# Kernel tuning notes

Hardware: AMD Instinct MI355X
Metric: run time of the kernel (lower is better)

The kernel has to match this reference:

```python
import jax, jax.numpy as jnp
import numpy as np

D = 512
H = 8
HD = D // H
EPS = 1e-5
NEG_INF = -1e30


def _ln(x, g, b):
    mu = jnp.mean(x, axis=-1, keepdims=True)
    var = jnp.mean(jnp.square(x - mu), axis=-1, keepdims=True)
    return (x - mu) * jax.lax.rsqrt(var + EPS) * g + b


def setup_inputs() -> dict:
    key = jax.random.key(0)
    ks = jax.random.split(key, 8)
    V, M, S = 128, 128, 514  # seq includes 2 head tokens (cls+dist)
    inp = {
        "video_embeds": jax.random.normal(ks[0], (V, D), jnp.float32),
        "music_features": jax.random.normal(ks[1], (M, S, D), jnp.float32),
        "music_masks": jnp.ones((M, S - 2), jnp.int32),
    }
    wk = jax.random.split(ks[2], 5)
    for name, k in zip(["Wq", "Wk", "Wv", "Wo", "Wl"], wk):
        inp[name] = jax.random.normal(k, (D, D), jnp.float32) * 0.02
    for name in ["bq", "bk", "bv", "bo", "bl"]:
        inp[name] = jnp.zeros((D,), jnp.float32)
    for name in ["g1", "g2", "g3"]:
        inp[name] = jnp.ones((D,), jnp.float32)
    for name in ["b1", "b2", "b3"]:
        inp[name] = jnp.zeros((D,), jnp.float32)
    return inp


def reference(video_embeds, music_features, music_masks,
              Wq, bq, Wk, bk, Wv, bv, Wo, bo, Wl, bl,
              g1, b1, g2, b2, g3, b3):
    # drop cls + dist tokens
    mf = music_features[:, 2:, :]  # (M, f, D)
    ve = _ln(video_embeds, g1, b1)  # (V, D)
    mf = _ln(mf, g1, b1)
    V = ve.shape[0]
    M, f, _ = mf.shape

    q = (ve @ Wq.T + bq).reshape(V, H, HD).transpose(1, 0, 2)        # (H, V, hd)
    k = (mf @ Wk.T + bk).reshape(M, f, H, HD).transpose(0, 2, 1, 3)  # (M, H, f, hd)
    v = (mf @ Wv.T + bv).reshape(M, f, H, HD).transpose(0, 2, 1, 3)  # (M, H, f, hd)

    logits = jnp.einsum('hvd,mhfd->vmhf', q, k) / np.sqrt(HD).astype(np.float32)
    mask = music_masks[None, :, None, :]  # (1, M, 1, f)
    logits = jnp.where(mask == 0, NEG_INF, logits)
    w = jax.nn.softmax(logits, axis=-1)
    attn = jnp.einsum('vmhf,mhfd->vmhd', w, v).reshape(V, M, D)
    attn = attn @ Wo.T + bo

    attn = _ln(attn, g2, b2)
    out = attn + (attn @ Wl.T + bl)  # dropout = identity in eval
    return _ln(out, g3, b3)
```

## Files before the change

kernel.cpp:

```cpp
#include <hip/hip_runtime.h>
#include <hip/hip_bf16.h>

typedef unsigned int uint;
typedef unsigned short ushort;
typedef __bf16 bf16;
typedef bf16 bf16x8 __attribute__((ext_vector_type(8)));
typedef float f32x4 __attribute__((ext_vector_type(4)));
typedef ushort ushort4v __attribute__((ext_vector_type(4)));

__device__ __forceinline__ float bf2f(ushort u) {
  union { uint u; float f; } v; v.u = ((uint)u) << 16; return v.f;
}
__device__ __forceinline__ ushort f2bf(float f) {
  union { float f; uint u; } v; v.f = f;
  uint u = v.u;
  uint r = (u + 0x7fffu + ((u >> 16) & 1u)) >> 16;
  return (ushort)r;
}

__device__ __forceinline__ void gl2lds16(const void* g, void* l) {
  __builtin_amdgcn_global_load_lds(
      (const __attribute__((address_space(1))) void*)g,
      (__attribute__((address_space(3))) void*)l, 16, 0, 0);
}

__device__ __forceinline__ void ln_rows0(
    int nrows, int blk, int nblk, int tid,
    const float* __restrict__ srcA,
    const float* __restrict__ g, const float* __restrict__ b,
    ushort* __restrict__ dst)
{
  const int l = tid & 63;
  const int nw = nblk * 4;
  for (int row = blk * 4 + (tid >> 6); row < nrows; row += nw) {
    const float* s = srcA + (size_t)row * 512;
    float x[8];
    float4 a0 = *(const float4*)(s + l * 4);
    float4 a1 = *(const float4*)(s + 256 + l * 4);
    x[0] = a0.x; x[1] = a0.y; x[2] = a0.z; x[3] = a0.w;
    x[4] = a1.x; x[5] = a1.y; x[6] = a1.z; x[7] = a1.w;
    float sum = 0.f, sq = 0.f;
    #pragma unroll
    for (int j = 0; j < 8; ++j) { sum += x[j]; sq += x[j] * x[j]; }
    #pragma unroll
    for (int o = 1; o < 64; o <<= 1) {
      sum += __shfl_xor(sum, o);
      sq  += __shfl_xor(sq, o);
    }
    float mu = sum * (1.f / 512.f);
    float var = sq * (1.f / 512.f) - mu * mu;
    float rstd = rsqrtf(var + 1e-5f);
    float4 g0 = *(const float4*)(g + l * 4);
    float4 g1 = *(const float4*)(g + 256 + l * 4);
    float4 b0 = *(const float4*)(b + l * 4);
    float4 b1 = *(const float4*)(b + 256 + l * 4);
    float gv[8] = {g0.x,g0.y,g0.z,g0.w,g1.x,g1.y,g1.z,g1.w};
    float bv[8] = {b0.x,b0.y,b0.z,b0.w,b1.x,b1.y,b1.z,b1.w};
    ushort* d = dst + (size_t)row * 512;
    ushort4v p0, p1;
    #pragma unroll
    for (int j = 0; j < 4; ++j) {
      p0[j] = f2bf((x[j] - mu) * rstd * gv[j] + bv[j]);
      p1[j] = f2bf((x[4+j] - mu) * rstd * gv[4+j] + bv[4+j]);
    }
    *(ushort4v*)(d + l * 4) = p0;
    *(ushort4v*)(d + 256 + l * 4) = p1;
  }
}

__device__ __forceinline__ void ln_pair1(
    int wid, int tid,
    const float* __restrict__ srcA,
    const float* __restrict__ g, const float* __restrict__ b,
    ushort* __restrict__ dst)
{
  const int l = tid & 63;
  const int r0 = wid * 2, r1 = r0 + 1;
  float x0[8], x1[8];
  int mm0 = r0 >> 9, fi0 = r0 & 511;
  int mm1 = r1 >> 9, fi1 = r1 & 511;
  const float* s0 = srcA + ((size_t)mm0 * 514 + 2 + fi0) * 512;
  const float* s1 = srcA + ((size_t)mm1 * 514 + 2 + fi1) * 512;
  float4 a0 = *(const float4*)(s0 + l * 4);
  float4 a1 = *(const float4*)(s0 + 256 + l * 4);
  float4 c0 = *(const float4*)(s1 + l * 4);
  float4 c1 = *(const float4*)(s1 + 256 + l * 4);
  x0[0]=a0.x; x0[1]=a0.y; x0[2]=a0.z; x0[3]=a0.w;
  x0[4]=a1.x; x0[5]=a1.y; x0[6]=a1.z; x0[7]=a1.w;
  x1[0]=c0.x; x1[1]=c0.y; x1[2]=c0.z; x1[3]=c0.w;
  x1[4]=c1.x; x1[5]=c1.y; x1[6]=c1.z; x1[7]=c1.w;
  float s0v = 0.f, q0 = 0.f, s1v = 0.f, q1 = 0.f;
  #pragma unroll
  for (int j = 0; j < 8; ++j) {
    s0v += x0[j]; q0 += x0[j] * x0[j];
    s1v += x1[j]; q1 += x1[j] * x1[j];
  }
  #pragma unroll
  for (int o = 1; o < 64; o <<= 1) {
    s0v += __shfl_xor(s0v, o); q0 += __shfl_xor(q0, o);
    s1v += __shfl_xor(s1v, o); q1 += __shfl_xor(q1, o);
  }
  float mu0 = s0v * (1.f/512.f), mu1 = s1v * (1.f/512.f);
  float rstd0 = rsqrtf(q0 * (1.f/512.f) - mu0 * mu0 + 1e-5f);
  float rstd1 = rsqrtf(q1 * (1.f/512.f) - mu1 * mu1 + 1e-5f);
  float4 g0 = *(const float4*)(g + l * 4);
  float4 g1v = *(const float4*)(g + 256 + l * 4);
  float4 b0 = *(const float4*)(b + l * 4);
  float4 b1v = *(const float4*)(b + 256 + l * 4);
  float gv[8] = {g0.x,g0.y,g0.z,g0.w,g1v.x,g1v.y,g1v.z,g1v.w};
  float bv[8] = {b0.x,b0.y,b0.z,b0.w,b1v.x,b1v.y,b1v.z,b1v.w};
  ushort* d0 = dst + (size_t)r0 * 512;
  ushort* d1 = dst + (size_t)r1 * 512;
  ushort4v p00, p01, p10, p11;
  #pragma unroll
  for (int j = 0; j < 4; ++j) {
    p00[j] = f2bf((x0[j]-mu0)*rstd0*gv[j]+bv[j]);
    p01[j] = f2bf((x0[4+j]-mu0)*rstd0*gv[4+j]+bv[4+j]);
    p10[j] = f2bf((x1[j]-mu1)*rstd1*gv[j]+bv[j]);
    p11[j] = f2bf((x1[4+j]-mu1)*rstd1*gv[4+j]+bv[4+j]);
  }
  *(ushort4v*)(d0 + l * 4) = p00;
  *(ushort4v*)(d0 + 256 + l * 4) = p01;
  *(ushort4v*)(d1 + l * 4) = p10;
  *(ushort4v*)(d1 + 256 + l * 4) = p11;
}

struct PreArgs {
  const float* s0; const float* s1; const float* s2; const float* s3; const float* s4;
  ushort* d0; ushort* d1; ushort* d2; ushort* d3; ushort* d4;
  const float* video; const float* music;
  const float* g1; const float* b1;
  ushort* veln; ushort* mfln;
};
__global__ __launch_bounds__(256) void preamble(PreArgs a) {
  int bb = blockIdx.x;
  if (bb < 640) {
    int t = bb * 256 + threadIdx.x;
    int which = t >> 15;
    int e = (t & 32767) * 8;
    const float* s = which == 0 ? a.s0 : which == 1 ? a.s1 : which == 2 ? a.s2 : which == 3 ? a.s3 : a.s4;
    ushort*      d = which == 0 ? a.d0 : which == 1 ? a.d1 : which == 2 ? a.d2 : which == 3 ? a.d3 : a.d4;
    float4 v0 = *(const float4*)(s + e);
    float4 v1 = *(const float4*)(s + e + 4);
    uint4 o;
    o.x = (uint)f2bf(v0.x) | ((uint)f2bf(v0.y) << 16);
    o.y = (uint)f2bf(v0.z) | ((uint)f2bf(v0.w) << 16);
    o.z = (uint)f2bf(v1.x) | ((uint)f2bf(v1.y) << 16);
    o.w = (uint)f2bf(v1.z) | ((uint)f2bf(v1.w) << 16);
    *(uint4*)(d + e) = o;
  } else if (bb < 672) {
    ln_rows0(128, bb - 640, 32, threadIdx.x, a.video, a.g1, a.b1, a.veln);
  } else {
    ln_pair1((bb - 672) * 4 + (threadIdx.x >> 6), threadIdx.x,
             a.music, a.g1, a.b1, a.mfln);
  }
}

__global__ __launch_bounds__(512) void gemm_kvq(
    const ushort* __restrict__ Amf, const ushort* __restrict__ Aq,
    const ushort* __restrict__ Wk, const ushort* __restrict__ Wv,
    const ushort* __restrict__ Wq,
    const float* __restrict__ bk, const float* __restrict__ bv,
    const float* __restrict__ bq,
    ushort* __restrict__ K, ushort* __restrict__ Vt, ushort* __restrict__ Q)
{
  __shared__ __align__(16) ushort As[2][256 * 64];
  __shared__ __align__(16) ushort Bks[2][128 * 64];
  __shared__ __align__(16) ushort Bvs[2][128 * 64];
  const int tid = threadIdx.x;
  const int w = tid >> 6, l = tid & 63;
  const int lg = l >> 4, lr = l & 15;
  const int wr = w >> 1, wc = w & 1;

  const bool isq = (blockIdx.y == 256);
  const int row0 = isq ? 0 : blockIdx.y * 256;
  const int col0 = blockIdx.x * 128;
  const ushort* Ap  = isq ? Aq : Amf;
  const ushort* Wkp = isq ? Wq : Wk;

  f32x4 kacc[4][4], vacc[4][4];
  #pragma unroll
  for (int i = 0; i < 4; i++)
    #pragma unroll
    for (int j = 0; j < 4; j++) {
      f32x4 z = {0.f,0.f,0.f,0.f};
      kacc[i][j] = z; vacc[i][j] = z;
    }

  size_t asrc[4], wksrc[2]; int aldst[4], wldst[2];
  {
    int r = tid >> 3, j = tid & 7;
    int koff = (j ^ (r & 7)) * 8;
    #pragma unroll
    for (int c2 = 0; c2 < 4; ++c2) {
      asrc[c2] = (size_t)(row0 + c2 * 64 + r) * 512 + koff;
      aldst[c2] = ((c2 * 64 + w * 8) * 64);
    }
    #pragma unroll
    for (int c2 = 0; c2 < 2; ++c2) {
      wksrc[c2] = (size_t)(col0 + c2 * 64 + r) * 512 + koff;
      wldst[c2] = ((c2 * 64 + w * 8) * 64);
    }
  }

  auto stage = [&](int pb, int kk) {
    #pragma unroll
    for (int c2 = 0; c2 < 4; ++c2)
      gl2lds16(Ap + asrc[c2] + kk * 64, &As[pb][aldst[c2]]);
    #pragma unroll
    for (int c2 = 0; c2 < 2; ++c2) {
      gl2lds16(Wkp + wksrc[c2] + kk * 64, &Bks[pb][wldst[c2]]);
      gl2lds16(Wv + wksrc[c2] + kk * 64, &Bvs[pb][wldst[c2]]);
    }
  };
  auto compute = [&](int pb) {
    #pragma unroll
    for (int ks = 0; ks < 2; ++ks) {
      bf16x8 af[4], bkf[4];
      #pragma unroll
      for (int mi = 0; mi < 4; ++mi) {
        int r = wr * 64 + mi * 16 + lr;
        af[mi] = *(const bf16x8*)(&As[pb][r * 64 + ((ks * 32 + lg * 8) ^ ((r & 7) * 8))]);
      }
      #pragma unroll
      for (int ni = 0; ni < 4; ++ni) {
        int r = wc * 64 + ni * 16 + lr;
        bkf[ni] = *(const bf16x8*)(&Bks[pb][r * 64 + ((ks * 32 + lg * 8) ^ ((r & 7) * 8))]);
      }
      #pragma unroll
      for (int mi = 0; mi < 4; ++mi)
        #pragma unroll
        for (int ni = 0; ni < 4; ++ni)
          kacc[mi][ni] = __builtin_amdgcn_mfma_f32_16x16x32_bf16(af[mi], bkf[ni], kacc[mi][ni], 0, 0, 0);
      if (!isq) {
        bf16x8 bvf[4];
        #pragma unroll
        for (int ni = 0; ni < 4; ++ni) {
          int r = wc * 64 + ni * 16 + lr;
          bvf[ni] = *(const bf16x8*)(&Bvs[pb][r * 64 + ((ks * 32 + lg * 8) ^ ((r & 7) * 8))]);
        }
        #pragma unroll
        for (int mi = 0; mi < 4; ++mi)
          #pragma unroll
          for (int ni = 0; ni < 4; ++ni)
            vacc[mi][ni] = __builtin_amdgcn_mfma_f32_16x16x32_bf16(af[mi], bvf[ni], vacc[mi][ni], 0, 0, 0);
      }
    }
  };

  stage(0, 0);
  __syncthreads();
  int cur = 0;
  #pragma unroll
  for (int kk = 0; kk < 7; ++kk) {
    stage(cur ^ 1, kk + 1);
    compute(cur);
    __syncthreads();
    cur ^= 1;
  }
  compute(cur);

  #pragma unroll
  for (int ni = 0; ni < 4; ++ni) {
    int cg = col0 + wc * 64 + ni * 16 + lr;
    float bkc = isq ? bq[cg] : bk[cg];
    float bvc = isq ? 0.f : bv[cg];
    #pragma unroll
    for (int mi = 0; mi < 4; ++mi) {
      int rg0 = row0 + wr * 64 + mi * 16 + lg * 4;
      if (isq) {
        if (rg0 < 128) {
          #pragma unroll
          for (int e = 0; e < 4; ++e)
            Q[(size_t)(rg0 + e) * 512 + cg] = f2bf((kacc[mi][ni][e] + bkc) * 0.125f);
        }
      } else {
        #pragma unroll
        for (int e = 0; e < 4; ++e)
          K[(size_t)(rg0 + e) * 512 + cg] = f2bf(kacc[mi][ni][e] + bkc);
        int m = rg0 >> 9, fi = rg0 & 511;
        ushort4v pk;
        #pragma unroll
        for (int e = 0; e < 4; ++e) pk[e] = f2bf(vacc[mi][ni][e] + bvc);
        *(ushort4v*)(Vt + (size_t)(m * 512 + cg) * 512 + fi) = pk;
      }
    }
  }
}

__global__ __launch_bounds__(512) void gemm_ln(
    const ushort* __restrict__ A, const ushort* __restrict__ W,
    const float* __restrict__ bias,
    const float* __restrict__ gam, const float* __restrict__ bet,
    void* __restrict__ outp, const ushort* __restrict__ resid, int outf32)
{
  __shared__ __align__(16) ushort As[2][64 * 64];
  __shared__ __align__(16) ushort Bs[2][512 * 64];
  __shared__ float red[8][64][2];
  const int tid = threadIdx.x;
  const int w = tid >> 6, l = tid & 63;
  const int lg = l >> 4, lr = l & 15;
  const int row0 = blockIdx.x * 64;

  f32x4 acc[4][4];
  #pragma unroll
  for (int i = 0; i < 4; i++)
    #pragma unroll
    for (int j = 0; j < 4; j++) { f32x4 z = {0.f,0.f,0.f,0.f}; acc[i][j] = z; }

  size_t asrc, wsrc0; int aldst;
  {
    int r = tid >> 3, j = tid & 7;
    int koff = (j ^ (r & 7)) * 8;
    asrc = (size_t)(row0 + r) * 512 + koff;
    wsrc0 = (size_t)r * 512 + koff;
    aldst = (w * 8) * 64;
  }

  auto stage = [&](int pb, int kk) {
    gl2lds16(A + asrc + kk * 64, &As[pb][aldst]);
    #pragma unroll
    for (int b = 0; b < 8; ++b)
      gl2lds16(W + wsrc0 + (size_t)b * 32768 + kk * 64,
               &Bs[pb][(b * 64 + w * 8) * 64]);
  };
  auto compute = [&](int pb) {
    #pragma unroll
    for (int ks = 0; ks < 2; ++ks) {
      bf16x8 af[4], bfr[4];
      #pragma unroll
      for (int mi = 0; mi < 4; ++mi) {
        int ra = mi * 16 + lr;
        af[mi] = *(const bf16x8*)(&As[pb][ra * 64 + ((ks * 32 + lg * 8) ^ ((ra & 7) * 8))]);
      }
      #pragma unroll
      for (int ni = 0; ni < 4; ++ni) {
        int rb = w * 64 + ni * 16 + lr;
        bfr[ni] = *(const bf16x8*)(&Bs[pb][rb * 64 + ((ks * 32 + lg * 8) ^ ((rb & 7) * 8))]);
      }
      __builtin_amdgcn_s_setprio(1);
      #pragma unroll
      for (int mi = 0; mi < 4; ++mi)
        #pragma unroll
        for (int ni = 0; ni < 4; ++ni)
          acc[mi][ni] = __builtin_amdgcn_mfma_f32_16x16x32_bf16(af[mi], bfr[ni], acc[mi][ni], 0, 0, 0);
      __builtin_amdgcn_s_setprio(0);
    }
  };

  stage(0, 0);
  __syncthreads();
  int cur = 0;
  #pragma unroll
  for (int kk = 0; kk < 7; ++kk) {
    stage(cur ^ 1, kk + 1);
    compute(cur);
    __syncthreads();
    cur ^= 1;
  }
  compute(cur);

  float bc[4], gv[4], bv2[4];
  #pragma unroll
  for (int ni = 0; ni < 4; ++ni) {
    int col = w * 64 + ni * 16 + lr;
    bc[ni] = bias[col];
    gv[ni] = gam[col];
    bv2[ni] = bet[col];
  }
  #pragma unroll
  for (int mi = 0; mi < 4; ++mi)
    #pragma unroll
    for (int e = 0; e < 4; ++e) {
      int row = row0 + mi * 16 + lg * 4 + e;
      #pragma unroll
      for (int ni = 0; ni < 4; ++ni) {
        float v = acc[mi][ni][e] + bc[ni];
        if (resid) v += bf2f(resid[(size_t)row * 512 + w * 64 + ni * 16 + lr]);
        acc[mi][ni][e] = v;
      }
    }
  #pragma unroll
  for (int mi = 0; mi < 4; ++mi)
    #pragma unroll
    for (int e = 0; e < 4; ++e) {
      float s = acc[mi][0][e] + acc[mi][1][e] + acc[mi][2][e] + acc[mi][3][e];
      float q = acc[mi][0][e]*acc[mi][0][e] + acc[mi][1][e]*acc[mi][1][e]
              + acc[mi][2][e]*acc[mi][2][e] + acc[mi][3][e]*acc[mi][3][e];
      #pragma unroll
      for (int o = 1; o < 16; o <<= 1) { s += __shfl_xor(s, o); q += __shfl_xor(q, o); }
      if (lr == 0) {
        int row = mi * 16 + lg * 4 + e;
        red[w][row][0] = s;
        red[w][row][1] = q;
      }
    }
  __syncthreads();
  #pragma unroll
  for (int mi = 0; mi < 4; ++mi)
    #pragma unroll
    for (int e = 0; e < 4; ++e) {
      int row = mi * 16 + lg * 4 + e;
      float S = 0.f, Qm = 0.f;
      #pragma unroll
      for (int w2 = 0; w2 < 8; ++w2) { S += red[w2][row][0]; Qm += red[w2][row][1]; }
      float mu = S * (1.f / 512.f);
      float var = Qm * (1.f / 512.f) - mu * mu;
      float rstd = rsqrtf(var + 1e-5f);
      int grow = row0 + row;
      if (!outf32) {
        ushort* o = (ushort*)outp;
        #pragma unroll
        for (int ni = 0; ni < 4; ++ni)
          o[(size_t)grow * 512 + w * 64 + ni * 16 + lr] =
              f2bf((acc[mi][ni][e] - mu) * rstd * gv[ni] + bv2[ni]);
      } else {
        float* o = (float*)outp;
        #pragma unroll
        for (int ni = 0; ni < 4; ++ni)
          o[(size_t)grow * 512 + w * 64 + ni * 16 + lr] =
              (acc[mi][ni][e] - mu) * rstd * gv[ni] + bv2[ni];
      }
    }
}

__global__ __launch_bounds__(256) void attn_kernel(
    const ushort* __restrict__ q, const ushort* __restrict__ k,
    const ushort* __restrict__ vt, const int* __restrict__ masks,
    ushort* __restrict__ attn)
{
  __shared__ __align__(16) ushort Qs[128 * 64];
  __shared__ __align__(16) ushort Ks[2][64 * 64];
  __shared__ __align__(16) ushort Vs[2][64 * 64];
  __shared__ __align__(16) ushort Ps[4][32 * 64];
  __shared__ float maskf[2][64];
  __shared__ float stats[4][32];

  const int tid = threadIdx.x;
  const int w = tid >> 6, l = tid & 63;
  const int lg = l >> 4, lr = l & 15;
  const int m = blockIdx.x >> 3, h = blockIdx.x & 7;

  const size_t kbase = (size_t)(m * 512) * 512 + h * 64;
  const size_t vbase = (size_t)(m * 512 + h * 64) * 512;

  auto stageKV = [&](int pb, int it) {
    const int f0 = it * 64;
    #pragma unroll
    for (int c2 = 0; c2 < 2; ++c2) {
      int c = c2 * 256 + tid;
      int r = c >> 3, j = c & 7;
      int off = (j * 8) ^ ((r & 7) * 8);
      gl2lds16(k + kbase + (size_t)(f0 + r) * 512 + off, &Ks[pb][(c2 * 256 + w * 64) * 8]);
      gl2lds16(vt + vbase + (size_t)r * 512 + f0 + off, &Vs[pb][(c2 * 256 + w * 64) * 8]);
    }
    if (tid < 64) maskf[pb][tid] = masks[m * 512 + f0 + tid] ? 0.f : -1e30f;
  };

  #pragma unroll
  for (int c2 = 0; c2 < 4; ++c2) {
    int c = c2 * 256 + tid;
    int r = c >> 3, j = c & 7;
    gl2lds16(q + (size_t)r * 512 + h * 64 + ((j * 8) ^ ((r & 7) * 8)),
             Qs + (c2 * 256 + w * 64) * 8);
  }
  stageKV(0, 0);
  __syncthreads();

  f32x4 acc[2][4];
  #pragma unroll
  for (int i = 0; i < 2; i++)
    #pragma unroll
    for (int j = 0; j < 4; j++) { f32x4 z = {0.f,0.f,0.f,0.f}; acc[i][j] = z; }
  float m_run[2] = {-INFINITY, -INFINITY};
  float l_run[2] = {0.f, 0.f};
  bf16x8 qf[2][2];
  #pragma unroll
  for (int nv = 0; nv < 2; ++nv)
    #pragma unroll
    for (int k2 = 0; k2 < 2; ++k2) {
      int v = w * 32 + nv * 16 + lr;
      qf[nv][k2] = *(const bf16x8*)(Qs + v * 64 + ((k2 * 32 + lg * 8) ^ ((v & 7) * 8)));
    }

  int cur = 0;
  for (int it = 0; it < 8; ++it) {
    if (it < 7) stageKV(cur ^ 1, it + 1);

    f32x4 s[4][2];
    #pragma unroll
    for (int mi = 0; mi < 4; mi++)
      #pragma unroll
      for (int nv = 0; nv < 2; nv++) { f32x4 z = {0.f,0.f,0.f,0.f}; s[mi][nv] = z; }
    #pragma unroll
    for (int k2 = 0; k2 < 2; ++k2) {
      bf16x8 kf[4];
      #pragma unroll
      for (int mi = 0; mi < 4; ++mi) {
        int f = mi * 16 + lr;
        kf[mi] = *(const bf16x8*)(&Ks[cur][f * 64 + ((k2 * 32 + lg * 8) ^ ((f & 7) * 8))]);
      }
      __builtin_amdgcn_s_setprio(1);
      #pragma unroll
      for (int mi = 0; mi < 4; ++mi)
        #pragma unroll
        for (int nv = 0; nv < 2; ++nv)
          s[mi][nv] = __builtin_amdgcn_mfma_f32_16x16x32_bf16(kf[mi], qf[nv][k2], s[mi][nv], 0, 0, 0);
      __builtin_amdgcn_s_setprio(0);
    }

    float mk[4][4];
    #pragma unroll
    for (int mi = 0; mi < 4; mi++)
      #pragma unroll
      for (int e = 0; e < 4; e++) mk[mi][e] = maskf[cur][mi * 16 + lg * 4 + e];

    #pragma unroll
    for (int nv = 0; nv < 2; ++nv) {
      float pmax = -INFINITY;
      #pragma unroll
      for (int mi = 0; mi < 4; mi++)
        #pragma unroll
        for (int e = 0; e < 4; e++) {
          s[mi][nv][e] += mk[mi][e];
          pmax = fmaxf(pmax, s[mi][nv][e]);
        }
      pmax = fmaxf(pmax, __shfl_xor(pmax, 16));
      pmax = fmaxf(pmax, __shfl_xor(pmax, 32));
      bool skip = __all(pmax - m_run[nv] <= 8.f);
      float mnew = skip ? m_run[nv] : fmaxf(m_run[nv], pmax);
      float sc = skip ? 1.f : __expf(m_run[nv] - mnew);
      float csum = 0.f;
      int vloc = nv * 16 + lr;
      #pragma unroll
      for (int mi = 0; mi < 4; mi++) {
        ushort4v pk;
        #pragma unroll
        for (int e = 0; e < 4; e++) {
          float p = __expf(s[mi][nv][e] - mnew);
          csum += p;
          pk[e] = f2bf(p);
        }
        int f = mi * 16 + lg * 4;
        *(ushort4v*)(&Ps[w][vloc * 64 + (f ^ ((vloc & 7) * 8))]) = pk;
      }
      csum += __shfl_xor(csum, 16);
      csum += __shfl_xor(csum, 32);
      l_run[nv] = l_run[nv] * sc + csum;
      m_run[nv] = mnew;
      if (lg == 0) stats[w][vloc] = sc;
      if (!skip) {
        int mi2 = nv;
        #pragma unroll
        for (int e = 0; e < 4; ++e) {
          float scv = stats[w][mi2 * 16 + lg * 4 + e];
          #pragma unroll
          for (int nd = 0; nd < 4; ++nd) acc[mi2][nd][e] *= scv;
        }
      }
    }

    #pragma unroll
    for (int k2 = 0; k2 < 2; ++k2) {
      bf16x8 pf[2], vf[4];
      #pragma unroll
      for (int mi2 = 0; mi2 < 2; ++mi2) {
        int vloc = mi2 * 16 + lr;
        pf[mi2] = *(const bf16x8*)(&Ps[w][vloc * 64 + ((k2 * 32 + lg * 8) ^ ((vloc & 7) * 8))]);
      }
      #pragma unroll
      for (int nd = 0; nd < 4; ++nd) {
        int d = nd * 16 + lr;
        vf[nd] = *(const bf16x8*)(&Vs[cur][d * 64 + ((k2 * 32 + lg * 8) ^ ((d & 7) * 8))]);
      }
      __builtin_amdgcn_s_setprio(1);
      #pragma unroll
      for (int mi2 = 0; mi2 < 2; ++mi2)
        #pragma unroll
        for (int nd = 0; nd < 4; ++nd)
          acc[mi2][nd] = __builtin_amdgcn_mfma_f32_16x16x32_bf16(pf[mi2], vf[nd], acc[mi2][nd], 0, 0, 0);
      __builtin_amdgcn_s_setprio(0);
    }
    __syncthreads();
    cur ^= 1;
  }

  #pragma unroll
  for (int nv = 0; nv < 2; ++nv)
    if (lg == 0) stats[w][nv * 16 + lr] = 1.f / l_run[nv];
  #pragma unroll
  for (int mi2 = 0; mi2 < 2; ++mi2)
    #pragma unroll
    for (int e = 0; e < 4; ++e) {
      float invl = stats[w][mi2 * 16 + lg * 4 + e];
      int vg = w * 32 + mi2 * 16 + lg * 4 + e;
      #pragma unroll
      for (int nd = 0; nd < 4; ++nd) {
        int d = nd * 16 + lr;
        attn[(size_t)(vg * 128 + m) * 512 + h * 64 + d] = f2bf(acc[mi2][nd][e] * invl);
      }
    }
}

extern "C" void kernel_launch(void* const* d_in, const int* in_sizes, int n_in,
                              void* d_out, int out_size, void* d_ws, size_t ws_size,
                              hipStream_t stream) {
  const float* video = (const float*)d_in[0];
  const float* music = (const float*)d_in[1];
  const int*   masks = (const int*)d_in[2];
  const float* Wq = (const float*)d_in[3];
  const float* Wk = (const float*)d_in[4];
  const float* Wv = (const float*)d_in[5];
  const float* Wo = (const float*)d_in[6];
  const float* Wl = (const float*)d_in[7];
  const float* bq = (const float*)d_in[8];
  const float* bk = (const float*)d_in[9];
  const float* bv = (const float*)d_in[10];
  const float* bo = (const float*)d_in[11];
  const float* bl = (const float*)d_in[12];
  const float* g1 = (const float*)d_in[13];
  const float* g2 = (const float*)d_in[14];
  const float* g3 = (const float*)d_in[15];
  const float* b1 = (const float*)d_in[16];
  const float* b2 = (const float*)d_in[17];
  const float* b3 = (const float*)d_in[18];

  char* ws = (char*)d_ws;
  ushort* mfln = (ushort*)(ws);
  ushort* kbuf = (ushort*)(ws + 67108864);
  ushort* vtb  = (ushort*)(ws + 134217728);
  ushort* attn = (ushort*)(ws + 201326592);
  ushort* xbuf = (ushort*)(ws + 234881024);
  ushort* veln = (ushort*)(ws + 251658240);
  ushort* qbuf = (ushort*)(ws + 251789312);
  ushort* wqb  = (ushort*)(ws + 251920384);
  ushort* wkb  = wqb + 262144;
  ushort* wvb  = wkb + 262144;
  ushort* wob  = wvb + 262144;
  ushort* wlb  = wob + 262144;

  PreArgs pa = {Wq, Wk, Wv, Wo, Wl, wqb, wkb, wvb, wob, wlb,
                video, music, g1, b1, veln, mfln};
  preamble<<<8864, 256, 0, stream>>>(pa);

  gemm_kvq<<<dim3(4, 257), 512, 0, stream>>>(
      mfln, veln, wkb, wvb, wqb, bk, bv, bq, kbuf, vtb, qbuf);

  attn_kernel<<<1024, 256, 0, stream>>>(qbuf, kbuf, vtb, masks, attn);

  gemm_ln<<<256, 512, 0, stream>>>(attn, wob, bo, g2, b2, xbuf, nullptr, 0);
  gemm_ln<<<256, 512, 0, stream>>>(xbuf, wlb, bl, g3, b3, d_out, xbuf, 1);
}
```

Before: 266.1 us.

## Halve K-tile in fused KVQ GEMM, remap block order, add MFMA priority hints

Shrinks the K-step of the fused K/V/Q projection GEMM from 64 to 32, which halves LDS use per block and lets more blocks stay resident per CU. The swizzle and staging are reworked to match, and the loop now runs 16 steps instead of 8. Blocks are reordered so consecutive blocks share the same weight column tile, and s_setprio is raised around the MFMA bursts. The trade-off is twice as many barriers and pipeline iterations, each with less work to overlap.

```diff
diff --git a/kernel.cpp b/kernel.cpp
--- a/kernel.cpp
+++ b/kernel.cpp
@@ -164,17 +164,20 @@
     const float* __restrict__ bq,
     ushort* __restrict__ K, ushort* __restrict__ Vt, ushort* __restrict__ Q)
 {
-  __shared__ __align__(16) ushort As[2][256 * 64];
-  __shared__ __align__(16) ushort Bks[2][128 * 64];
-  __shared__ __align__(16) ushort Bvs[2][128 * 64];
+  __shared__ __align__(16) ushort As[2][256 * 32];
+  __shared__ __align__(16) ushort Bks[2][128 * 32];
+  __shared__ __align__(16) ushort Bvs[2][128 * 32];
   const int tid = threadIdx.x;
   const int w = tid >> 6, l = tid & 63;
   const int lg = l >> 4, lr = l & 15;
   const int wr = w >> 1, wc = w & 1;
 
-  const bool isq = (blockIdx.y == 256);
-  const int row0 = isq ? 0 : blockIdx.y * 256;
-  const int col0 = blockIdx.x * 128;
+  const int flat = blockIdx.y * 4 + blockIdx.x;
+  const bool isq = (flat >= 1024);
+  const int xb = isq ? (flat - 1024) : (flat >> 8);
+  const int yb = isq ? 0 : (flat & 255);
+  const int row0 = yb * 256;
+  const int col0 = xb * 128;
   const ushort* Ap  = isq ? Aq : Amf;
   const ushort* Wkp = isq ? Wq : Wk;
 
@@ -187,64 +190,65 @@
       kacc[i][j] = z; vacc[i][j] = z;
     }
 
-  size_t asrc[4], wksrc[2]; int aldst[4], wldst[2];
+  size_t asrc[2], wsrc; int aldst[2], wldst;
   {
-    int r = tid >> 3, j = tid & 7;
-    int koff = (j ^ (r & 7)) * 8;
-    #pragma unroll
-    for (int c2 = 0; c2 < 4; ++c2) {
-      asrc[c2] = (size_t)(row0 + c2 * 64 + r) * 512 + koff;
-      aldst[c2] = ((c2 * 64 + w * 8) * 64);
-    }
-    #pragma unroll
-    for (int c2 = 0; c2 < 2; ++c2) {
-      wksrc[c2] = (size_t)(col0 + c2 * 64 + r) * 512 + koff;
-      wldst[c2] = ((c2 * 64 + w * 8) * 64);
-    }
+    int j = tid & 3;
+    #pragma unroll
+    for (int i = 0; i < 2; ++i) {
+      int r = i * 128 + (tid >> 2);
+      int koff = (j ^ ((r >> 1) & 3)) * 8;
+      asrc[i] = (size_t)(row0 + r) * 512 + koff;
+      aldst[i] = i * 4096 + w * 512;
+    }
+    int r = tid >> 2;
+    int koff = (j ^ ((r >> 1) & 3)) * 8;
+    wsrc = (size_t)(col0 + r) * 512 + koff;
+    wldst = w * 512;
   }
 
   auto stage = [&](int pb, int kk) {
     #pragma unroll
-    for (int c2 = 0; c2 < 4; ++c2)
-      gl2lds16(Ap + asrc[c2] + kk * 64, &As[pb][aldst[c2]]);
-    #pragma unroll
-    for (int c2 = 0; c2 < 2; ++c2) {
-      gl2lds16(Wkp + wksrc[c2] + kk * 64, &Bks[pb][wldst[c2]]);
-      gl2lds16(Wv + wksrc[c2] + kk * 64, &Bvs[pb][wldst[c2]]);
-    }
+    for (int i = 0; i < 2; ++i)
+      gl2lds16(Ap + asrc[i] + kk * 32, &As[pb][aldst[i]]);
+    gl2lds16(Wkp + wsrc + kk * 32, &Bks[pb][wldst]);
+    gl2lds16(Wv + wsrc + kk * 32, &Bvs[pb][wldst]);
   };
   auto compute = [&](int pb) {
-    #pragma unroll
-    for (int ks = 0; ks < 2; ++ks) {
-      bf16x8 af[4], bkf[4];
-      #pragma unroll
-      for (int mi = 0; mi < 4; ++mi) {
-        int r = wr * 64 + mi * 16 + lr;
-        af[mi] = *(const bf16x8*)(&As[pb][r * 64 + ((ks * 32 + lg * 8) ^ ((r & 7) * 8))]);
-      }
+    bf16x8 af[4], bkf[4];
+    #pragma unroll
+    for (int mi = 0; mi < 4; ++mi) {
+      int r = wr * 64 + mi * 16 + lr;
+      int c = lg ^ ((r >> 1) & 3);
+      af[mi] = *(const bf16x8*)(&As[pb][r * 32 + c * 8]);
+    }
+    #pragma unroll
+    for (int ni = 0; ni < 4; ++ni) {
+      int r = wc * 64 + ni * 16 + lr;
+      int c = lg ^ ((r >> 1) & 3);
+      bkf[ni] = *(const bf16x8*)(&Bks[pb][r * 32 + c * 8]);
+    }
+    __builtin_amdgcn_s_setprio(1);
+    #pragma unroll
+    for (int mi = 0; mi < 4; ++mi)
+      #pragma unroll
+      for (int ni = 0; ni < 4; ++ni)
+        kacc[mi][ni] = __builtin_amdgcn_mfma_f32_16x16x32_bf16(af[mi], bkf[ni], kacc[mi][ni], 0, 0, 0);
+    __builtin_amdgcn_s_setprio(0);
+    if (!isq) {
+      bf16x8 bvf[4];
       #pragma unroll
       for (int ni = 0; ni < 4; ++ni) {
         int r = wc * 64 + ni * 16 + lr;
-        bkf[ni] = *(const bf16x8*)(&Bks[pb][r * 64 + ((ks * 32 + lg * 8) ^ ((r & 7) * 8))]);
-      }
+        int c = lg ^ ((r >> 1) & 3);
+        bvf[ni] = *(const bf16x8*)(&Bvs[pb][r * 32 + c * 8]);
+      }
+      __builtin_amdgcn_s_setprio(1);
       #pragma unroll
       for (int mi = 0; mi < 4; ++mi)
         #pragma unroll
         for (int ni = 0; ni < 4; ++ni)
-          kacc[mi][ni] = __builtin_amdgcn_mfma_f32_16x16x32_bf16(af[mi], bkf[ni], kacc[mi][ni], 0, 0, 0);
-      if (!isq) {
-        bf16x8 bvf[4];
-        #pragma unroll
-        for (int ni = 0; ni < 4; ++ni) {
-          int r = wc * 64 + ni * 16 + lr;
-          bvf[ni] = *(const bf16x8*)(&Bvs[pb][r * 64 + ((ks * 32 + lg * 8) ^ ((r & 7) * 8))]);
-        }
-        #pragma unroll
-        for (int mi = 0; mi < 4; ++mi)
-          #pragma unroll
-          for (int ni = 0; ni < 4; ++ni)
-            vacc[mi][ni] = __builtin_amdgcn_mfma_f32_16x16x32_bf16(af[mi], bvf[ni], vacc[mi][ni], 0, 0, 0);
-      }
+          vacc[mi][ni] = __builtin_amdgcn_mfma_f32_16x16x32_bf16(af[mi], bvf[ni], vacc[mi][ni], 0, 0, 0);
+      __builtin_amdgcn_s_setprio(0);
     }
   };
 
@@ -252,7 +256,7 @@
   __syncthreads();
   int cur = 0;
   #pragma unroll
-  for (int kk = 0; kk < 7; ++kk) {
+  for (int kk = 0; kk < 15; ++kk) {
     stage(cur ^ 1, kk + 1);
     compute(cur);
     __syncthreads();
```

Measured after the change: 282.4 us. +6.1%, slower.
